# Performance work log

Hardware: AMD Instinct MI355X
Metric: run time of the kernel (lower is better)

The kernel has to match this reference:

```python
import jax, jax.numpy as jnp
import numpy as np

KB = 0.0019872041      # Boltzmann constant, kcal/(mol*K)
TEMP = 300.0
ALPHA = 10.0
BW = 0.15              # Gaussian KDE bandwidth
PAIR_I = jnp.array([0, 0, 0, 1, 1, 2])
PAIR_J = jnp.array([1, 2, 3, 2, 3, 3])

B, N_ATOMS = 512, 1024
G, L, K, D = 256, 8, 128, 6


def setup_inputs() -> dict:
    key = jax.random.key(0)
    k1, k2, k3, k4, k5, k6 = jax.random.split(key, 6)
    positions = jax.random.normal(k1, (B, N_ATOMS, 3), dtype=jnp.float32) * 2.0
    # KDE training samples live in 6-dim distance space (positive, few Angstroms)
    kde_samples = jax.random.uniform(k2, (G, L, K, D), dtype=jnp.float32) * 5.0
    weight = jax.random.uniform(k3, (G, L), dtype=jnp.float32)
    offset = jax.random.normal(k4, (G, L), dtype=jnp.float32)
    atom_idxs = jax.random.randint(k5, (G, L, 4), 0, N_ATOMS)
    group_sizes = jax.random.randint(k6, (G,), 0, L)  # clamped to >=1 in reference
    return {"positions": positions, "kde_samples": kde_samples, "weight": weight,
            "offset": offset, "atom_idxs": atom_idxs, "group_sizes": group_sizes}


def reference(positions, kde_samples, weight, offset, atom_idxs, group_sizes):
    Gn, Ln, Kn, Dn = kde_samples.shape
    # Gather the 4 vertices of every loss: [B, G, L, 4, 3]
    vp = positions[:, atom_idxs]
    # 6 pairwise distances per loss: [B, G, L, 6]
    diff = vp[..., PAIR_I, :] - vp[..., PAIR_J, :]
    dists = jnp.sqrt(jnp.sum(diff * diff, axis=-1) + 1e-12)
    # Gaussian KDE log-density over the K training samples, expanded squared
    x2 = jnp.sum(dists * dists, axis=-1)          # [B,G,L]
    mu2 = jnp.sum(kde_samples * kde_samples, -1)  # [G,L,K]
    xmu = jnp.einsum('bgld,glkd->bglk', dists, kde_samples)
    sq = x2[..., None] + mu2[None] - 2.0 * xmu    # [B,G,L,K]
    log_norm = jnp.log(jnp.float32(Kn)) + 0.5 * Dn * jnp.log(2.0 * jnp.pi * BW * BW)
    logP = jax.nn.logsumexp(-sq / (2.0 * BW * BW), axis=-1) - log_norm  # [B,G,L]
    energy = -KB * TEMP * logP
    scaled = energy * weight + offset             # [B,G,L]
    # Ragged group reduction: min over the valid losses of each group
    sizes = jnp.maximum(group_sizes, 1)
    mask = jnp.arange(Ln)[None, :] < sizes[:, None]        # [G,L]
    group_min = jnp.min(jnp.where(mask, scaled, jnp.inf), axis=-1)  # [B,G]
    # soft-min across groups
    return -jax.nn.logsumexp(-ALPHA * group_min, axis=-1) / ALPHA   # [B]
```

## Files before the change

kernel.cpp:

```cpp
#include <hip/hip_runtime.h>

#define NB 512
#define NATOMS 1024
#define NG 256
#define NL 8
#define NK 128

#define KBT 0.59616123f
#define ALPHA_C 10.0f
#define LN2 0.6931471805599453f
#define LOG2E 1.4426950408889634f
#define INV2BW2 22.222221f
#define SCALE2 (INV2BW2 * LOG2E)
#define LOG_NORM (-1.0170649f)

#define WL_CAP 2048
#define FILL_BLOCKS 128

typedef _Float16 f16x8 __attribute__((ext_vector_type(8)));
typedef float f32x16 __attribute__((ext_vector_type(16)));

__device__ __forceinline__ float fexp2(float x) { return __builtin_amdgcn_exp2f(x); }
__device__ __forceinline__ float flog2(float x) { return __builtin_amdgcn_logf(x); }

__device__ __forceinline__ unsigned fkey(float f) {
  unsigned u = __float_as_uint(f);
  return (u & 0x80000000u) ? ~u : (u | 0x80000000u);
}
__device__ __forceinline__ float funkey(unsigned k) {
  unsigned u = (k & 0x80000000u) ? (k ^ 0x80000000u) : ~k;
  return __uint_as_float(u);
}

__device__ __forceinline__ float wred_min(float v) {
#pragma unroll
  for (int m = 32; m >= 1; m >>= 1) v = fminf(v, __shfl_xor(v, m, 64));
  return v;
}
__device__ __forceinline__ float wred_sum(float v) {
#pragma unroll
  for (int m = 32; m >= 1; m >>= 1) v += __shfl_xor(v, m, 64);
  return v;
}

__global__ __launch_bounds__(256) void prep_small(
    const int* __restrict__ gsizes, int* __restrict__ wl,
    uint4* __restrict__ gmin_u4) {
  const int t = threadIdx.x;
  if (blockIdx.x != 0) {
    const unsigned F = 0xFFFFFFFFu;
    gmin_u4[(blockIdx.x - 1) * 256 + t] = make_uint4(F, F, F, F);
    return;
  }
  const int lane = t & 63, wid = t >> 6;
  int gs = gsizes[t];
  int nl = gs < 1 ? 1 : (gs > NL ? NL : gs);
  int x = nl;
#pragma unroll
  for (int m = 1; m < 64; m <<= 1) {
    int y = __shfl_up(x, m, 64);
    if (lane >= m) x += y;
  }
  __shared__ int wsum[4];
  if (lane == 63) wsum[wid] = x;
  __syncthreads();
  int off = 0;
  for (int i = 0; i < wid; ++i) off += wsum[i];
  int inc = off + x, exc = inc - nl;
  for (int j = 0; j < nl; ++j) wl[exc + j] = (t << 3) | j;
  if (t == 255) wl[WL_CAP] = inc;
}

__global__ __launch_bounds__(256) void stage1_kernel(
    const float* __restrict__ positions, const float* __restrict__ kde,
    const float* __restrict__ weight, const float* __restrict__ offs,
    const int* __restrict__ atom_idxs, const int* __restrict__ wl,
    unsigned* __restrict__ gmin_u) {
  const int count = wl[WL_CAP];
  const int w = blockIdx.x >> 2;
  if (w >= count) return;
  const int gl = wl[w];
  const int g = gl >> 3;

  const int t = threadIdx.x;
  const int lane = t & 63;
  const int col = lane & 31, h = lane >> 5;
  const int b = ((blockIdx.x & 3) << 7) + ((t >> 6) << 5) + col;

  __shared__ f16x8 tabL[8][64];

  const int4 idx = *reinterpret_cast<const int4*>(atom_idxs + (gl << 2));
  const int ids[4] = {idx.x, idx.y, idx.z, idx.w};
  const float* pb = positions + (size_t)b * NATOMS * 3;
  float ax[4], ay[4], az[4];
#pragma unroll
  for (int j = 0; j < 4; ++j) {
    const float3 p = *reinterpret_cast<const float3*>(pb + ids[j] * 3);
    ax[j] = p.x; ay[j] = p.y; az[j] = p.z;
  }

  if (t < NK) {
    const float* mp = kde + ((size_t)gl * NK + t) * 6;
    float mu2 = 0.0f;
    _Float16 ah[6], al[6];
#pragma unroll
    for (int q = 0; q < 6; ++q) {
      float mv = mp[q];
      mu2 += mv * mv;
      float a = (2.0f * SCALE2) * mv;
      _Float16 hh = (_Float16)a;
      ah[q] = hh;
      al[q] = (_Float16)(a - (float)hh);
    }
    float z = -SCALE2 * mu2;
    _Float16 z1 = (_Float16)z;
    _Float16 z2 = (_Float16)(z - (float)z1);
    const _Float16 Z = (_Float16)0.0f;
    const int kt = t >> 5, m = t & 31;
    tabL[kt * 2 + 0][m]      = (f16x8){ah[0],ah[1],ah[2],ah[3],ah[4],ah[5],al[0],al[1]};
    tabL[kt * 2 + 0][m + 32] = (f16x8){al[2],al[3],al[4],al[5],ah[0],ah[1],ah[2],ah[3]};
    tabL[kt * 2 + 1][m]      = (f16x8){ah[4],ah[5],al[0],al[1],al[2],al[3],al[4],al[5]};
    tabL[kt * 2 + 1][m + 32] = (f16x8){z1,  z2,  Z,   Z,   Z,   Z,   Z,   Z   };
  }

  const int PI_[6] = {0, 0, 0, 1, 1, 2};
  const int PJ_[6] = {1, 2, 3, 2, 3, 3};
  float d[6]; float x2 = 0.0f;
#pragma unroll
  for (int q = 0; q < 6; ++q) {
    float dx = ax[PI_[q]] - ax[PJ_[q]];
    float dy = ay[PI_[q]] - ay[PJ_[q]];
    float dz = az[PI_[q]] - az[PJ_[q]];
    float dd = dx * dx + dy * dy + dz * dz + 1e-12f;
    d[q] = sqrtf(dd);
    x2 += d[q] * d[q];
  }
  const float c2 = -x2 * SCALE2;

  _Float16 xh[6], xl[6];
#pragma unroll
  for (int q = 0; q < 6; ++q) {
    _Float16 hh = (_Float16)d[q];
    xh[q] = hh;
    xl[q] = (_Float16)(d[q] - (float)hh);
  }
  const _Float16 ONE = (_Float16)1.0f, Z = (_Float16)0.0f;
  f16x8 Bf0 = (h == 0)
    ? (f16x8){xh[0],xh[1],xh[2],xh[3],xh[4],xh[5],xh[0],xh[1]}
    : (f16x8){xh[2],xh[3],xh[4],xh[5],xl[0],xl[1],xl[2],xl[3]};
  f16x8 Bf1 = (h == 0)
    ? (f16x8){xl[4],xl[5],xl[0],xl[1],xl[2],xl[3],xl[4],xl[5]}
    : (f16x8){ONE,  ONE,  Z,   Z,   Z,   Z,   Z,   Z   };

  __syncthreads();

  const f32x16 zz = {0.0f};
  f32x16 acc[4];
#pragma unroll
  for (int kt = 0; kt < 4; ++kt) {
    f16x8 A0 = tabL[kt * 2 + 0][lane];
    f16x8 A1 = tabL[kt * 2 + 1][lane];
    acc[kt] = __builtin_amdgcn_mfma_f32_32x32x16_f16(
        A1, Bf1, __builtin_amdgcn_mfma_f32_32x32x16_f16(A0, Bf0, zz, 0, 0, 0),
        0, 0, 0);
  }

  float mkt[4];
#pragma unroll
  for (int kt = 0; kt < 4; ++kt) {
    float m0 = fmaxf(fmaxf(acc[kt][0], acc[kt][1]), fmaxf(acc[kt][2], acc[kt][3]));
    float m1 = fmaxf(fmaxf(acc[kt][4], acc[kt][5]), fmaxf(acc[kt][6], acc[kt][7]));
    float m2 = fmaxf(fmaxf(acc[kt][8], acc[kt][9]), fmaxf(acc[kt][10], acc[kt][11]));
    float m3 = fmaxf(fmaxf(acc[kt][12], acc[kt][13]), fmaxf(acc[kt][14], acc[kt][15]));
    mkt[kt] = fmaxf(fmaxf(m0, m1), fmaxf(m2, m3));
  }
  float mx = fmaxf(fmaxf(mkt[0], mkt[1]), fmaxf(mkt[2], mkt[3]));
  mx = fmaxf(mx, __shfl_xor(mx, 32, 64));

  float s0 = 0.0f, s1 = 0.0f, s2 = 0.0f, s3 = 0.0f;
#pragma unroll
  for (int kt = 0; kt < 4; ++kt) {
    s0 += fexp2(acc[kt][0] - mx)  + fexp2(acc[kt][1] - mx)
        + fexp2(acc[kt][2] - mx)  + fexp2(acc[kt][3] - mx);
    s1 += fexp2(acc[kt][4] - mx)  + fexp2(acc[kt][5] - mx)
        + fexp2(acc[kt][6] - mx)  + fexp2(acc[kt][7] - mx);
    s2 += fexp2(acc[kt][8] - mx)  + fexp2(acc[kt][9] - mx)
        + fexp2(acc[kt][10] - mx) + fexp2(acc[kt][11] - mx);
    s3 += fexp2(acc[kt][12] - mx) + fexp2(acc[kt][13] - mx)
        + fexp2(acc[kt][14] - mx) + fexp2(acc[kt][15] - mx);
  }
  float s = (s0 + s1) + (s2 + s3);
  s += __shfl_xor(s, 32, 64);

  if (h == 0) {
    float lse2 = c2 + mx + flog2(s);
    float logP = lse2 * LN2 - LOG_NORM;
    float scaled = -KBT * logP * weight[gl] + offs[gl];
    atomicMin(&gmin_u[g * NB + b], fkey(scaled));
  }
}

__global__ __launch_bounds__(256) void stage2_kernel(
    const unsigned* __restrict__ gmin_u, float* __restrict__ out) {
  const int b = blockIdx.x;
  const int t = threadIdx.x;
  const int lane = t & 63;
  const int wid = t >> 6;
  float v = funkey(gmin_u[t * NB + b]);
  __shared__ float sm[4], ss[4];
  float m = wred_min(v);
  if (lane == 0) sm[wid] = m;
  __syncthreads();
  float M = fminf(fminf(sm[0], sm[1]), fminf(sm[2], sm[3]));
  float e = fexp2(-ALPHA_C * LOG2E * (v - M));
  float s = wred_sum(e);
  if (lane == 0) ss[wid] = s;
  __syncthreads();
  if (t == 0) {
    float S = ss[0] + ss[1] + ss[2] + ss[3];
    out[b] = M - flog2(S) * LN2 / ALPHA_C;
  }
}

extern "C" void kernel_launch(void* const* d_in, const int* in_sizes, int n_in,
                              void* d_out, int out_size, void* d_ws, size_t ws_size,
                              hipStream_t stream) {
  const float* positions = (const float*)d_in[0];
  const float* kde       = (const float*)d_in[1];
  const float* weight    = (const float*)d_in[2];
  const float* offs      = (const float*)d_in[3];
  const int*   atom_idxs = (const int*)d_in[4];
  const int*   gsizes    = (const int*)d_in[5];
  float* out = (float*)d_out;

  unsigned* gmin_u = (unsigned*)d_ws;
  int* wl = (int*)d_ws + (size_t)NG * NB;

  prep_small<<<dim3(1 + FILL_BLOCKS), dim3(256), 0, stream>>>(
      gsizes, wl, (uint4*)gmin_u);
  stage1_kernel<<<dim3(WL_CAP * 4), dim3(256), 0, stream>>>(
      positions, kde, weight, offs, atom_idxs, wl, gmin_u);
  stage2_kernel<<<dim3(NB), dim3(256), 0, stream>>>(gmin_u, out);
}
```

Baseline: 35.85 us.

## Replace atomicMin group reduction with per-loss stores and ragged min in stage2

```diff
diff --git a/kernel.cpp b/kernel.cpp
--- a/kernel.cpp
+++ b/kernel.cpp
@@ -15,7 +15,6 @@
 #define LOG_NORM (-1.0170649f)
 
 #define WL_CAP 2048
-#define FILL_BLOCKS 128
 
 typedef _Float16 f16x8 __attribute__((ext_vector_type(8)));
 typedef float f32x16 __attribute__((ext_vector_type(16)));
@@ -23,15 +22,6 @@
 __device__ __forceinline__ float fexp2(float x) { return __builtin_amdgcn_exp2f(x); }
 __device__ __forceinline__ float flog2(float x) { return __builtin_amdgcn_logf(x); }
 
-__device__ __forceinline__ unsigned fkey(float f) {
-  unsigned u = __float_as_uint(f);
-  return (u & 0x80000000u) ? ~u : (u | 0x80000000u);
-}
-__device__ __forceinline__ float funkey(unsigned k) {
-  unsigned u = (k & 0x80000000u) ? (k ^ 0x80000000u) : ~k;
-  return __uint_as_float(u);
-}
-
 __device__ __forceinline__ float wred_min(float v) {
 #pragma unroll
   for (int m = 32; m >= 1; m >>= 1) v = fminf(v, __shfl_xor(v, m, 64));
@@ -43,15 +33,9 @@
   return v;
 }
 
-__global__ __launch_bounds__(256) void prep_small(
-    const int* __restrict__ gsizes, int* __restrict__ wl,
-    uint4* __restrict__ gmin_u4) {
+__global__ __launch_bounds__(256) void prep_wl(
+    const int* __restrict__ gsizes, int* __restrict__ wl) {
   const int t = threadIdx.x;
-  if (blockIdx.x != 0) {
-    const unsigned F = 0xFFFFFFFFu;
-    gmin_u4[(blockIdx.x - 1) * 256 + t] = make_uint4(F, F, F, F);
-    return;
-  }
   const int lane = t & 63, wid = t >> 6;
   int gs = gsizes[t];
   int nl = gs < 1 ? 1 : (gs > NL ? NL : gs);
@@ -75,12 +59,11 @@
     const float* __restrict__ positions, const float* __restrict__ kde,
     const float* __restrict__ weight, const float* __restrict__ offs,
     const int* __restrict__ atom_idxs, const int* __restrict__ wl,
-    unsigned* __restrict__ gmin_u) {
+    float* __restrict__ scaled_out) {
   const int count = wl[WL_CAP];
   const int w = blockIdx.x >> 2;
   if (w >= count) return;
   const int gl = wl[w];
-  const int g = gl >> 3;
 
   const int t = threadIdx.x;
   const int lane = t & 63;
@@ -195,18 +178,24 @@
   if (h == 0) {
     float lse2 = c2 + mx + flog2(s);
     float logP = lse2 * LN2 - LOG_NORM;
-    float scaled = -KBT * logP * weight[gl] + offs[gl];
-    atomicMin(&gmin_u[g * NB + b], fkey(scaled));
+    float sc = -KBT * logP * weight[gl] + offs[gl];
+    scaled_out[(size_t)gl * NB + b] = sc;
   }
 }
 
 __global__ __launch_bounds__(256) void stage2_kernel(
-    const unsigned* __restrict__ gmin_u, float* __restrict__ out) {
+    const float* __restrict__ scaled_in, const int* __restrict__ gsizes,
+    float* __restrict__ out) {
   const int b = blockIdx.x;
   const int t = threadIdx.x;
   const int lane = t & 63;
   const int wid = t >> 6;
-  float v = funkey(gmin_u[t * NB + b]);
+  int gs = gsizes[t];
+  int nl = gs < 1 ? 1 : (gs > NL ? NL : gs);
+  float v = 1e30f;
+  for (int l = 0; l < nl; ++l)
+    v = fminf(v, scaled_in[(size_t)((t << 3) + l) * NB + b]);
+
   __shared__ float sm[4], ss[4];
   float m = wred_min(v);
   if (lane == 0) sm[wid] = m;
@@ -233,12 +222,11 @@
   const int*   gsizes    = (const int*)d_in[5];
   float* out = (float*)d_out;
 
-  unsigned* gmin_u = (unsigned*)d_ws;
-  int* wl = (int*)d_ws + (size_t)NG * NB;
-
-  prep_small<<<dim3(1 + FILL_BLOCKS), dim3(256), 0, stream>>>(
-      gsizes, wl, (uint4*)gmin_u);
+  float* scaled = (float*)d_ws;
+  int* wl = (int*)((char*)d_ws + (4 << 20));
+
+  prep_wl<<<dim3(1), dim3(256), 0, stream>>>(gsizes, wl);
   stage1_kernel<<<dim3(WL_CAP * 4), dim3(256), 0, stream>>>(
-      positions, kde, weight, offs, atom_idxs, wl, gmin_u);
-  stage2_kernel<<<dim3(NB), dim3(256), 0, stream>>>(gmin_u, out);
-}
+      positions, kde, weight, offs, atom_idxs, wl, scaled);
+  stage2_kernel<<<dim3(NB), dim3(256), 0, stream>>>(scaled, gsizes, out);
+}
```

Result: slower. 38.71 us (+8.0%).
